# Kernel optimization log

Measured on AMD Instinct MI355X. Metric: run time of the kernel, lower is better.

The kernel has to match this reference:

```python
import jax, jax.numpy as jnp
import numpy as np

EPS = 0.05
N = 33554432  # 2**25 annotation steps


def setup_inputs() -> dict:
    key = jax.random.key(0)
    # categories in 1..5 (cat==0 is a no-op skip in the original loop; excluding it
    # keeps the output length static at N+1)
    annotation_series = jax.random.randint(key, (N,), 1, 6, dtype=jnp.int64 if jax.config.jax_enable_x64 else jnp.int32)
    # learned scalar weights of the six Linear(1,1,bias=False) layers, at their init constants
    return {
        "annotation_series": annotation_series,
        "origin_w": jnp.asarray(0.0, jnp.float32),
        "big_decrease_w": jnp.asarray(-0.3, jnp.float32),
        "decrease_w": jnp.asarray(-0.1, jnp.float32),
        "same_w": jnp.asarray(0.0, jnp.float32),
        "increase_w": jnp.asarray(0.1, jnp.float32),
        "big_increase_w": jnp.asarray(0.3, jnp.float32),
    }


def _change_table(origin_w, bd, d, s, inc, bi):
    sg = jax.lax.stop_gradient  # clamp bounds came from .item() in torch -> detached
    c1 = jnp.minimum(bd, sg(jnp.minimum(0.0, d))) - EPS                 # big decrease
    c2 = jnp.clip(d, sg(bd) + EPS, 0.0 - EPS)                           # decrease
    c3 = s                                                              # same
    c4 = jnp.clip(inc, 0.0 + EPS, sg(bi) - EPS)                         # increase
    c5 = jnp.maximum(bi, sg(jnp.maximum(0.0, inc)) + EPS)               # big increase
    zero = jnp.zeros_like(c1)  # cat 0 unused (inputs restricted to 1..5)
    return jnp.stack([zero, c1, c2, c3, c4, c5])  # [6]


def reference(annotation_series, origin_w, big_decrease_w, decrease_w, same_w, increase_w, big_increase_w):
    table = _change_table(origin_w, big_decrease_w, decrease_w, same_w, increase_w, big_increase_w)
    changes = table[annotation_series]                    # [N] gather from 6-entry LUT
    series = origin_w + jnp.cumsum(changes)               # [N] inclusive prefix sum
    return jnp.concatenate([origin_w[None], series])      # [N+1]
```

## Files before the change

### kernel.cpp

```cpp
#include <hip/hip_runtime.h>

#define EPS_C 0.05f
#define BLOCK 256
#define BPB   8192

typedef int i4 __attribute__((ext_vector_type(4)));
typedef float f4 __attribute__((ext_vector_type(4)));
typedef unsigned int u2 __attribute__((ext_vector_type(2)));

__device__ __forceinline__ void build_table(const float* bd_p, const float* d_p,
                                            const float* s_p, const float* inc_p,
                                            const float* bi_p, float* cs) {
  if (threadIdx.x == 0) {
    float bd = *bd_p, d = *d_p, s = *s_p, inc = *inc_p, bi = *bi_p;
    cs[0] = 0.0f;
    cs[1] = fminf(bd, fminf(0.0f, d)) - EPS_C;
    cs[2] = fminf(fmaxf(d, bd + EPS_C), -EPS_C);
    cs[3] = s;
    cs[4] = fminf(fmaxf(inc, EPS_C), bi - EPS_C);
    cs[5] = fmaxf(bi, fmaxf(0.0f, inc) + EPS_C);
    cs[6] = 0.0f; cs[7] = 0.0f;
  }
}

__global__ __launch_bounds__(BLOCK) void k_pack_reduce(
    const int* __restrict__ ann, const float* bd, const float* d,
    const float* s, const float* inc, const float* bi,
    u2* __restrict__ pack, float* __restrict__ coarse,
    float* __restrict__ fine) {
  __shared__ float cs[8];
  __shared__ float wsum[4];
  build_table(bd, d, s, inc, bi, cs);
  __syncthreads();
  const int t = threadIdx.x, lane = t & 63, w = t >> 6, b = blockIdx.x;
  const size_t ebase = (size_t)b * BPB + (size_t)w * 2048;
  const i4* in4 = (const i4*)ann + (ebase >> 2) + lane;
  float fs[2];
#pragma unroll
  for (int u = 0; u < 2; ++u) {
    unsigned lo = 0, hi = 0;
    float sum = 0.0f;
#pragma unroll
    for (int r = 0; r < 4; ++r) {
      i4 v = __builtin_nontemporal_load(&in4[u * 256 + r * 64]);
      sum += cs[v.x] + cs[v.y] + cs[v.z] + cs[v.w];
      unsigned nib = (unsigned)v.x | ((unsigned)v.y << 4) |
                     ((unsigned)v.z << 8) | ((unsigned)v.w << 12);
      if (r & 1) { if (r < 2) lo |= nib << 16; else hi |= nib << 16; }
      else       { if (r < 2) lo |= nib;       else hi |= nib; }
    }
    pack[((size_t)b * 8 + w * 2 + u) * 64 + lane] = (u2){lo, hi};
#pragma unroll
    for (int off = 32; off >= 1; off >>= 1) sum += __shfl_xor(sum, off, 64);
    fs[u] = sum;
  }
  if (lane == 0) {
    fine[b * 8 + w * 2 + 0] = fs[0];
    fine[b * 8 + w * 2 + 1] = fs[1];
    wsum[w] = fs[0] + fs[1];
  }
  __syncthreads();
  if (t == 0) coarse[b] = wsum[0] + wsum[1] + wsum[2] + wsum[3];
}

__global__ __launch_bounds__(BLOCK) void k_scan_out(
    const u2* __restrict__ pack, const float* __restrict__ coarse,
    const float* __restrict__ fine, const float* __restrict__ origin,
    const float* bd, const float* d, const float* s, const float* inc,
    const float* bi, float* __restrict__ out, int nb) {
  __shared__ float cs[8];
  __shared__ float ws2[4];
  build_table(bd, d, s, inc, bi, cs);
  const int t = threadIdx.x, lane = t & 63, w = t >> 6, b = blockIdx.x;

  const u2 pk0 = pack[((size_t)b * 8 + w * 2 + 0) * 64 + lane];
  const u2 pk1 = pack[((size_t)b * 8 + w * 2 + 1) * 64 + lane];

  float p = 0.0f;
  for (int i = t; i < b; i += BLOCK) p += coarse[i];
#pragma unroll
  for (int off = 32; off >= 1; off >>= 1) p += __shfl_xor(p, off, 64);
  if (lane == 0) ws2[w] = p;
  __syncthreads();
  const float P = *origin + ws2[0] + ws2[1] + ws2[2] + ws2[3];

  float f = (lane < 8) ? fine[b * 8 + lane] : 0.0f;
#pragma unroll
  for (int off = 1; off < 8; off <<= 1) {
    float y = __shfl_up(f, off, 64);
    if (lane >= off && lane < 8) f += y;
  }
  if (b == nb - 1 && w == 0 && lane == 7)
    out[(size_t)nb * BPB] = P + f;

  const u2 pks[2] = {pk0, pk1};
#pragma unroll
  for (int h = 0; h < 2; ++h) {
    const int j = w * 2 + h;
    float carry = P + ((j > 0) ? __shfl(f, j - 1, 64) : 0.0f);
    const u2 pk = pks[h];
    const size_t ubase = (size_t)b * BPB + (size_t)j * 1024;
#pragma unroll
    for (int r = 0; r < 4; ++r) {
      const unsigned pw = (r < 2) ? pk.x : pk.y;
      const unsigned us = (r & 1) ? (pw >> 16) : (pw & 0xFFFFu);
      const float v0 = cs[us & 0xFu];
      const float v1 = cs[(us >> 4) & 0xFu];
      const float v2 = cs[(us >> 8) & 0xFu];
      const float v3 = cs[(us >> 12) & 0xFu];
      const float s4 = v0 + v1 + v2 + v3;
      float x = s4;
#pragma unroll
      for (int off = 1; off < 64; off <<= 1) {
        float y = __shfl_up(x, off, 64);
        if (lane >= off) x += y;
      }
      const float off0 = carry + (x - s4);
      f4 o;
      o.x = off0;
      o.y = off0 + v0;
      o.z = o.y + v1;
      o.w = o.z + v2;
      __builtin_nontemporal_store(o, (f4*)(out + ubase + r * 256 + lane * 4));
      carry += __shfl(x, 63, 64);
    }
  }
}

extern "C" void kernel_launch(void* const* d_in, const int* in_sizes, int n_in,
                              void* d_out, int out_size, void* d_ws, size_t ws_size,
                              hipStream_t stream) {
  const int*   ann    = (const int*)d_in[0];
  const float* origin = (const float*)d_in[1];
  const float* bd     = (const float*)d_in[2];
  const float* dw     = (const float*)d_in[3];
  const float* sw     = (const float*)d_in[4];
  const float* ic     = (const float*)d_in[5];
  const float* bi     = (const float*)d_in[6];
  float* out = (float*)d_out;

  const int N  = in_sizes[0];
  const int nb = N / BPB;

  float* coarse = (float*)d_ws;
  float* fine   = coarse + 4096;
  u2*    pack   = (u2*)(fine + 32768);

  k_pack_reduce<<<nb, BLOCK, 0, stream>>>(ann, bd, dw, sw, ic, bi,
                                          pack, coarse, fine);
  k_scan_out<<<nb, BLOCK, 0, stream>>>(pack, coarse, fine, origin,
                                       bd, dw, sw, ic, bi, out, nb);
}
```

Measured before the change: 241.1 us.

## Drop nibble-packed intermediate and re-read cached annotations in scan kernel

The reduce kernel no longer writes a 4-bit packed copy of the annotations, and the scan kernel reads the original int32 annotations directly. Nontemporal loads become regular loads so the input may stay in the last-level cache between the two kernels. The scan kernel issues its input loads before the coarse prefix reduction and barrier to overlap latency. This trades the packed write and read for a second full-width read of the input, which costs more if it misses cache.

```diff
diff --git a/kernel.cpp b/kernel.cpp
--- a/kernel.cpp
+++ b/kernel.cpp
@@ -6,7 +6,6 @@
 
 typedef int i4 __attribute__((ext_vector_type(4)));
 typedef float f4 __attribute__((ext_vector_type(4)));
-typedef unsigned int u2 __attribute__((ext_vector_type(2)));
 
 __device__ __forceinline__ void build_table(const float* bd_p, const float* d_p,
                                             const float* s_p, const float* inc_p,
@@ -23,11 +22,10 @@
   }
 }
 
-__global__ __launch_bounds__(BLOCK) void k_pack_reduce(
+__global__ __launch_bounds__(BLOCK) void k_reduce(
     const int* __restrict__ ann, const float* bd, const float* d,
     const float* s, const float* inc, const float* bi,
-    u2* __restrict__ pack, float* __restrict__ coarse,
-    float* __restrict__ fine) {
+    float* __restrict__ coarse, float* __restrict__ fine) {
   __shared__ float cs[8];
   __shared__ float wsum[4];
   build_table(bd, d, s, inc, bi, cs);
@@ -38,18 +36,12 @@
   float fs[2];
 #pragma unroll
   for (int u = 0; u < 2; ++u) {
-    unsigned lo = 0, hi = 0;
     float sum = 0.0f;
 #pragma unroll
     for (int r = 0; r < 4; ++r) {
-      i4 v = __builtin_nontemporal_load(&in4[u * 256 + r * 64]);
+      i4 v = in4[u * 256 + r * 64];
       sum += cs[v.x] + cs[v.y] + cs[v.z] + cs[v.w];
-      unsigned nib = (unsigned)v.x | ((unsigned)v.y << 4) |
-                     ((unsigned)v.z << 8) | ((unsigned)v.w << 12);
-      if (r & 1) { if (r < 2) lo |= nib << 16; else hi |= nib << 16; }
-      else       { if (r < 2) lo |= nib;       else hi |= nib; }
     }
-    pack[((size_t)b * 8 + w * 2 + u) * 64 + lane] = (u2){lo, hi};
 #pragma unroll
     for (int off = 32; off >= 1; off >>= 1) sum += __shfl_xor(sum, off, 64);
     fs[u] = sum;
@@ -64,7 +56,7 @@
 }
 
 __global__ __launch_bounds__(BLOCK) void k_scan_out(
-    const u2* __restrict__ pack, const float* __restrict__ coarse,
+    const int* __restrict__ ann, const float* __restrict__ coarse,
     const float* __restrict__ fine, const float* __restrict__ origin,
     const float* bd, const float* d, const float* s, const float* inc,
     const float* bi, float* __restrict__ out, int nb) {
@@ -72,42 +64,45 @@
   __shared__ float ws2[4];
   build_table(bd, d, s, inc, bi, cs);
   const int t = threadIdx.x, lane = t & 63, w = t >> 6, b = blockIdx.x;
+  const size_t ebase = (size_t)b * BPB + (size_t)w * 2048;
+  const i4* in4 = (const i4*)ann + (ebase >> 2) + lane;
 
-  const u2 pk0 = pack[((size_t)b * 8 + w * 2 + 0) * 64 + lane];
-  const u2 pk1 = pack[((size_t)b * 8 + w * 2 + 1) * 64 + lane];
+  i4 v[8];
+#pragma unroll
+  for (int r = 0; r < 8; ++r) v[r] = in4[r * 64];
+  float f = (lane < 8) ? fine[b * 8 + lane] : 0.0f;
+  const float org = *origin;
 
   float p = 0.0f;
   for (int i = t; i < b; i += BLOCK) p += coarse[i];
 #pragma unroll
   for (int off = 32; off >= 1; off >>= 1) p += __shfl_xor(p, off, 64);
   if (lane == 0) ws2[w] = p;
-  __syncthreads();
-  const float P = *origin + ws2[0] + ws2[1] + ws2[2] + ws2[3];
 
-  float f = (lane < 8) ? fine[b * 8 + lane] : 0.0f;
 #pragma unroll
   for (int off = 1; off < 8; off <<= 1) {
     float y = __shfl_up(f, off, 64);
     if (lane >= off && lane < 8) f += y;
   }
+
+  __syncthreads();
+  const float P = org + ws2[0] + ws2[1] + ws2[2] + ws2[3];
+
   if (b == nb - 1 && w == 0 && lane == 7)
     out[(size_t)nb * BPB] = P + f;
 
-  const u2 pks[2] = {pk0, pk1};
 #pragma unroll
   for (int h = 0; h < 2; ++h) {
     const int j = w * 2 + h;
     float carry = P + ((j > 0) ? __shfl(f, j - 1, 64) : 0.0f);
-    const u2 pk = pks[h];
     const size_t ubase = (size_t)b * BPB + (size_t)j * 1024;
 #pragma unroll
     for (int r = 0; r < 4; ++r) {
-      const unsigned pw = (r < 2) ? pk.x : pk.y;
-      const unsigned us = (r & 1) ? (pw >> 16) : (pw & 0xFFFFu);
-      const float v0 = cs[us & 0xFu];
-      const float v1 = cs[(us >> 4) & 0xFu];
-      const float v2 = cs[(us >> 8) & 0xFu];
-      const float v3 = cs[(us >> 12) & 0xFu];
+      const i4 vv = v[h * 4 + r];
+      const float v0 = cs[vv.x];
+      const float v1 = cs[vv.y];
+      const float v2 = cs[vv.z];
+      const float v3 = cs[vv.w];
       const float s4 = v0 + v1 + v2 + v3;
       float x = s4;
 #pragma unroll
@@ -144,10 +139,8 @@
 
   float* coarse = (float*)d_ws;
   float* fine   = coarse + 4096;
-  u2*    pack   = (u2*)(fine + 32768);
 
-  k_pack_reduce<<<nb, BLOCK, 0, stream>>>(ann, bd, dw, sw, ic, bi,
-                                          pack, coarse, fine);
-  k_scan_out<<<nb, BLOCK, 0, stream>>>(pack, coarse, fine, origin,
+  k_reduce<<<nb, BLOCK, 0, stream>>>(ann, bd, dw, sw, ic, bi, coarse, fine);
+  k_scan_out<<<nb, BLOCK, 0, stream>>>(ann, coarse, fine, origin,
                                        bd, dw, sw, ic, bi, out, nb);
 }
```

After: 260.7 us. 8.1% more time.

## Fuse reduce and scan into one persistent pass with grid-wide barrier

Applied to the files above, without the earlier changes.

Replaces the two-kernel reduce-then-scan with a single kernel of 512 co-resident blocks. Each block keeps its packed annotation nibbles in registers, publishes its block sum, waits at a grid-wide barrier built from striped atomic counters, then computes its prefix and writes the output. This removes the workspace round-trip of the packed data and one kernel launch. It depends on all blocks being resident at once (checked with an occupancy query) and costs spin-wait time plus higher register pressure. The old two-kernel path remains as a fallback.

```diff
diff --git a/kernel.cpp b/kernel.cpp
--- a/kernel.cpp
+++ b/kernel.cpp
@@ -1,12 +1,17 @@
 #include <hip/hip_runtime.h>
 
 #define EPS_C 0.05f
-#define BLOCK 256
-#define BPB   8192
+#define BLOCK 512
+#define NBLK  512
+#define BPB   65536
+#define NCNT  32
 
 typedef int i4 __attribute__((ext_vector_type(4)));
 typedef float f4 __attribute__((ext_vector_type(4)));
-typedef unsigned int u2 __attribute__((ext_vector_type(2)));
+
+__global__ void k_zero(unsigned int* __restrict__ p) {
+  if (threadIdx.x < NCNT) p[threadIdx.x] = 0u;
+}
 
 __device__ __forceinline__ void build_table(const float* bd_p, const float* d_p,
                                             const float* s_p, const float* inc_p,
@@ -23,21 +28,25 @@
   }
 }
 
-__global__ __launch_bounds__(BLOCK) void k_pack_reduce(
-    const int* __restrict__ ann, const float* bd, const float* d,
-    const float* s, const float* inc, const float* bi,
-    u2* __restrict__ pack, float* __restrict__ coarse,
-    float* __restrict__ fine) {
+__global__ __launch_bounds__(BLOCK, 4) void k_onepass(
+    const int* __restrict__ ann, const float* __restrict__ origin,
+    const float* bd, const float* d, const float* s, const float* inc,
+    const float* bi, float* __restrict__ out, float* __restrict__ coarse,
+    unsigned int* __restrict__ cnt, int nb) {
   __shared__ float cs[8];
-  __shared__ float wsum[4];
+  __shared__ float wsum[8];
+  __shared__ float ws2[8];
+  const int t = threadIdx.x, lane = t & 63, w = t >> 6, b = blockIdx.x;
+
   build_table(bd, d, s, inc, bi, cs);
   __syncthreads();
-  const int t = threadIdx.x, lane = t & 63, w = t >> 6, b = blockIdx.x;
-  const size_t ebase = (size_t)b * BPB + (size_t)w * 2048;
+
+  const size_t ebase = (size_t)b * BPB + (size_t)w * 8192;
   const i4* in4 = (const i4*)ann + (ebase >> 2) + lane;
-  float fs[2];
-#pragma unroll
-  for (int u = 0; u < 2; ++u) {
+  unsigned pk[16];
+  float usum[8];
+#pragma unroll
+  for (int u = 0; u < 8; ++u) {
     unsigned lo = 0, hi = 0;
     float sum = 0.0f;
 #pragma unroll
@@ -49,7 +58,126 @@
       if (r & 1) { if (r < 2) lo |= nib << 16; else hi |= nib << 16; }
       else       { if (r < 2) lo |= nib;       else hi |= nib; }
     }
-    pack[((size_t)b * 8 + w * 2 + u) * 64 + lane] = (u2){lo, hi};
+    pk[u * 2] = lo; pk[u * 2 + 1] = hi;
+#pragma unroll
+    for (int off = 32; off >= 1; off >>= 1) sum += __shfl_xor(sum, off, 64);
+    usum[u] = sum;
+  }
+  float wtot = 0.0f;
+#pragma unroll
+  for (int u = 0; u < 8; ++u) wtot += usum[u];
+  if (lane == 0) wsum[w] = wtot;
+  const float org = *origin;
+  __syncthreads();
+  if (t == 0) {
+    float bt = 0.0f;
+#pragma unroll
+    for (int i = 0; i < 8; ++i) bt += wsum[i];
+    __hip_atomic_store(&coarse[b], bt, __ATOMIC_RELEASE,
+                       __HIP_MEMORY_SCOPE_AGENT);
+    __hip_atomic_fetch_add(&cnt[b & (NCNT - 1)], 1u, __ATOMIC_RELEASE,
+                           __HIP_MEMORY_SCOPE_AGENT);
+  }
+
+  if (w == 0) {
+    for (;;) {
+      unsigned c = (lane < NCNT)
+          ? __hip_atomic_load(&cnt[lane], __ATOMIC_ACQUIRE,
+                              __HIP_MEMORY_SCOPE_AGENT)
+          : 0u;
+#pragma unroll
+      for (int off = 32; off >= 1; off >>= 1) c += __shfl_xor(c, off, 64);
+      if (c == (unsigned)nb) break;
+      __builtin_amdgcn_s_sleep(8);
+    }
+  }
+  __syncthreads();
+
+  float p = (t < b) ? __hip_atomic_load(&coarse[t], __ATOMIC_RELAXED,
+                                        __HIP_MEMORY_SCOPE_AGENT)
+                    : 0.0f;
+#pragma unroll
+  for (int off = 32; off >= 1; off >>= 1) p += __shfl_xor(p, off, 64);
+  if (lane == 0) ws2[w] = p;
+  __syncthreads();
+  float P = org;
+#pragma unroll
+  for (int i = 0; i < 8; ++i) P += ws2[i];
+
+  float wexcl = 0.0f;
+#pragma unroll
+  for (int i = 0; i < 8; ++i) { float wv = wsum[i]; if (i < w) wexcl += wv; }
+
+  if (b == nb - 1 && w == 7 && lane == 0) {
+    float bt = wexcl;
+#pragma unroll
+    for (int u = 0; u < 8; ++u) bt += usum[u];
+    out[(size_t)nb * BPB] = P + bt;
+  }
+
+  float carry = P + wexcl;
+#pragma unroll
+  for (int u = 0; u < 8; ++u) {
+    float c2 = carry;
+#pragma unroll
+    for (int r = 0; r < 4; ++r) {
+      const unsigned pw = (r < 2) ? pk[u * 2] : pk[u * 2 + 1];
+      const unsigned us = (r & 1) ? (pw >> 16) : (pw & 0xFFFFu);
+      const float v0 = cs[us & 0xFu];
+      const float v1 = cs[(us >> 4) & 0xFu];
+      const float v2 = cs[(us >> 8) & 0xFu];
+      const float v3 = cs[(us >> 12) & 0xFu];
+      const float s4 = v0 + v1 + v2 + v3;
+      float x = s4;
+#pragma unroll
+      for (int off = 1; off < 64; off <<= 1) {
+        float y = __shfl_up(x, off, 64);
+        if (lane >= off) x += y;
+      }
+      const float off0 = c2 + (x - s4);
+      f4 o;
+      o.x = off0;
+      o.y = off0 + v0;
+      o.z = o.y + v1;
+      o.w = o.z + v2;
+      __builtin_nontemporal_store(
+          o, (f4*)(out + ebase + u * 1024 + r * 256 + lane * 4));
+      c2 += __shfl(x, 63, 64);
+    }
+    carry += usum[u];
+  }
+}
+
+
+typedef unsigned int uu2 __attribute__((ext_vector_type(2)));
+
+__global__ __launch_bounds__(256) void k_pack_reduce(
+    const int* __restrict__ ann, const float* bd, const float* d,
+    const float* s, const float* inc, const float* bi,
+    uu2* __restrict__ pack, float* __restrict__ coarse,
+    float* __restrict__ fine) {
+  __shared__ float cs[8];
+  __shared__ float wsum[4];
+  build_table(bd, d, s, inc, bi, cs);
+  __syncthreads();
+  const int t = threadIdx.x, lane = t & 63, w = t >> 6, b = blockIdx.x;
+  const size_t ebase = (size_t)b * 8192 + (size_t)w * 2048;
+  const i4* in4 = (const i4*)ann + (ebase >> 2) + lane;
+  float fs[2];
+#pragma unroll
+  for (int u = 0; u < 2; ++u) {
+    unsigned lo = 0, hi = 0;
+    float sum = 0.0f;
+#pragma unroll
+    for (int r = 0; r < 4; ++r) {
+      i4 v = __builtin_nontemporal_load(&in4[u * 256 + r * 64]);
+      sum += cs[v.x] + cs[v.y] + cs[v.z] + cs[v.w];
+      unsigned nib = (unsigned)v.x | ((unsigned)v.y << 4) |
+                     ((unsigned)v.z << 8) | ((unsigned)v.w << 12);
+      if (r & 1) { if (r < 2) lo |= nib << 16; else hi |= nib << 16; }
+      else       { if (r < 2) lo |= nib;       else hi |= nib; }
+    }
+    pack[((size_t)b * 8 + w * 2 + u) * 64 + lane] = (uu2){lo, hi};
 #pragma unroll
     for (int off = 32; off >= 1; off >>= 1) sum += __shfl_xor(sum, off, 64);
     fs[u] = sum;
@@ -63,8 +191,8 @@
   if (t == 0) coarse[b] = wsum[0] + wsum[1] + wsum[2] + wsum[3];
 }
 
-__global__ __launch_bounds__(BLOCK) void k_scan_out(
-    const u2* __restrict__ pack, const float* __restrict__ coarse,
+__global__ __launch_bounds__(256) void k_scan_out(
+    const uu2* __restrict__ pack, const float* __restrict__ coarse,
     const float* __restrict__ fine, const float* __restrict__ origin,
     const float* bd, const float* d, const float* s, const float* inc,
     const float* bi, float* __restrict__ out, int nb) {
@@ -73,33 +201,36 @@
   build_table(bd, d, s, inc, bi, cs);
   const int t = threadIdx.x, lane = t & 63, w = t >> 6, b = blockIdx.x;
 
-  const u2 pk0 = pack[((size_t)b * 8 + w * 2 + 0) * 64 + lane];
-  const u2 pk1 = pack[((size_t)b * 8 + w * 2 + 1) * 64 + lane];
+  const uu2 pk0 = pack[((size_t)b * 8 + w * 2 + 0) * 64 + lane];
+  const uu2 pk1 = pack[((size_t)b * 8 + w * 2 + 1) * 64 + lane];
+  float f = (lane < 8) ? fine[b * 8 + lane] : 0.0f;
+  const float org = *origin;
 
   float p = 0.0f;
-  for (int i = t; i < b; i += BLOCK) p += coarse[i];
+  for (int i = t; i < b; i += 256) p += coarse[i];
 #pragma unroll
   for (int off = 32; off >= 1; off >>= 1) p += __shfl_xor(p, off, 64);
   if (lane == 0) ws2[w] = p;
-  __syncthreads();
-  const float P = *origin + ws2[0] + ws2[1] + ws2[2] + ws2[3];
-
-  float f = (lane < 8) ? fine[b * 8 + lane] : 0.0f;
+
 #pragma unroll
   for (int off = 1; off < 8; off <<= 1) {
     float y = __shfl_up(f, off, 64);
     if (lane >= off && lane < 8) f += y;
   }
+
+  __syncthreads();
+  const float P = org + ws2[0] + ws2[1] + ws2[2] + ws2[3];
+
   if (b == nb - 1 && w == 0 && lane == 7)
-    out[(size_t)nb * BPB] = P + f;
-
-  const u2 pks[2] = {pk0, pk1};
+    out[(size_t)nb * 8192] = P + f;
+
+  const uu2 pks[2] = {pk0, pk1};
 #pragma unroll
   for (int h = 0; h < 2; ++h) {
     const int j = w * 2 + h;
     float carry = P + ((j > 0) ? __shfl(f, j - 1, 64) : 0.0f);
-    const u2 pk = pks[h];
-    const size_t ubase = (size_t)b * BPB + (size_t)j * 1024;
+    const uu2 pk = pks[h];
+    const size_t ubase = (size_t)b * 8192 + (size_t)j * 1024;
 #pragma unroll
     for (int r = 0; r < 4; ++r) {
       const unsigned pw = (r < 2) ? pk.x : pk.y;
@@ -139,15 +270,28 @@
   const float* bi     = (const float*)d_in[6];
   float* out = (float*)d_out;
 
-  const int N  = in_sizes[0];
-  const int nb = N / BPB;
+  const int N = in_sizes[0];
 
   float* coarse = (float*)d_ws;
-  float* fine   = coarse + 4096;
-  u2*    pack   = (u2*)(fine + 32768);
-
-  k_pack_reduce<<<nb, BLOCK, 0, stream>>>(ann, bd, dw, sw, ic, bi,
-                                          pack, coarse, fine);
-  k_scan_out<<<nb, BLOCK, 0, stream>>>(pack, coarse, fine, origin,
-                                       bd, dw, sw, ic, bi, out, nb);
-}
+  unsigned int* cnt = (unsigned int*)(coarse + 4096);
+  float* fine = (float*)(cnt + NCNT);
+  uu2* pack = (uu2*)(fine + 32768);
+
+  if (N == NBLK * BPB) {
+    int maxb = 0;
+    hipError_t qe = hipOccupancyMaxActiveBlocksPerMultiprocessor(
+        &maxb, (const void*)k_onepass, BLOCK, 0);
+    if (qe == hipSuccess && maxb >= 2) {
+      k_zero<<<1, 64, 0, stream>>>(cnt);
+      k_onepass<<<NBLK, BLOCK, 0, stream>>>(ann, origin, bd, dw, sw, ic, bi,
+                                            out, coarse, cnt, NBLK);
+      return;
+    }
+  }
+
+  const int nb = N / 8192;
+  k_pack_reduce<<<nb, 256, 0, stream>>>(ann, bd, dw, sw, ic, bi,
+                                        pack, coarse, fine);
+  k_scan_out<<<nb, 256, 0, stream>>>(pack, coarse, fine, origin,
+                                     bd, dw, sw, ic, bi, out, nb);
+}
```

Result: no change. 241.5 us (+0.2%).
